# Kernel tuning notes

Measured on AMD Instinct MI355X. Metric: run time of the kernel, lower is better.

Reference implementation:

```python
import jax, jax.numpy as jnp
import numpy as np

E = 8        # num_experts
D = 512      # embed_size
H = 8        # attention heads
HD = D // H  # head dim
B, S = 4, 1024


def setup_inputs() -> dict:
    key = jax.random.key(0)
    ks = jax.random.split(key, 16)
    sd = 0.02
    return {
        "x":  jax.random.normal(ks[0], (B, S, D), jnp.float32),
        # per-expert FFN params, stacked over expert dim
        "W1": jax.random.normal(ks[1], (E, D, 4 * D), jnp.float32) * sd,
        "b1": jnp.zeros((E, 4 * D), jnp.float32),
        "W2": jax.random.normal(ks[2], (E, 4 * D, D), jnp.float32) * sd,
        "b2": jnp.zeros((E, D), jnp.float32),
        # MultiheadAttention in_proj (split) and out_proj
        "Wq": jax.random.normal(ks[3], (D, D), jnp.float32) * sd,
        "bq": jnp.zeros((D,), jnp.float32),
        "Wk": jax.random.normal(ks[4], (D, D), jnp.float32) * sd,
        "bk": jnp.zeros((D,), jnp.float32),
        "Wv": jax.random.normal(ks[5], (D, D), jnp.float32) * sd,
        "bv": jnp.zeros((D,), jnp.float32),
        "Wo": jax.random.normal(ks[6], (D, D), jnp.float32) * sd,
        "bo": jnp.zeros((D,), jnp.float32),
        "expert_id": 3,
    }


def reference(x, W1, b1, W2, b2, Wq, bq, Wk, bk, Wv, bv, Wo, bo, expert_id):
    # --- batched per-expert FFN (fuses the Python loop over experts) ---
    # hidden: [B, E, S, 4D]
    hidden = jax.nn.relu(jnp.einsum('bsd,edf->besf', x, W1) + b1[None, :, None, :])
    eo = jnp.einsum('besf,efd->besd', hidden, W2) + b2[None, :, None, :]  # [B,E,S,D]
    eo = eo.transpose(0, 2, 1, 3)  # [B, S, E, D]

    Bs, Ss = x.shape[0], x.shape[1]
    a = eo.reshape(Bs * Ss, E, D)  # [N, E, D]; attention runs over the expert dim

    # --- MultiheadAttention (batch_first), torch semantics ---
    # NOTE: the original passes a FLOAT tril-of-ones attn_mask, which torch ADDS
    # to the scores (it does NOT mask with -inf). We reproduce that faithfully.
    q = (a @ Wq.T + bq).reshape(-1, E, H, HD).transpose(0, 2, 1, 3)  # [N,H,E,hd]
    k = (a @ Wk.T + bk).reshape(-1, E, H, HD).transpose(0, 2, 1, 3)
    v = (a @ Wv.T + bv).reshape(-1, E, H, HD).transpose(0, 2, 1, 3)

    mask = jnp.tril(jnp.ones((E, E), jnp.float32))  # additive float mask
    scores = jnp.einsum('nhed,nhfd->nhef', q, k) / jnp.sqrt(jnp.float32(HD))
    scores = scores + mask[None, None, :, :]
    attn = jax.nn.softmax(scores, axis=-1)
    ctx = jnp.einsum('nhef,nhfd->nhed', attn, v)           # [N,H,E,hd]
    ctx = ctx.transpose(0, 2, 1, 3).reshape(-1, E, D)       # [N,E,D]
    out = ctx @ Wo.T + bo                                   # [N,E,D]

    out = out.reshape(Bs, Ss, E, D)
    return out[:, :, expert_id, :]  # [B, S, D]
```

## Files before the change

kernel.cpp:

```cpp
#include <hip/hip_runtime.h>
#include <hip/hip_bf16.h>

typedef __hip_bfloat16 bf16;
typedef __attribute__((ext_vector_type(4))) float f32x4;
typedef __attribute__((ext_vector_type(8))) short s16x8;

#define N_TOK 4096
#define Dm    512
#define Fm    2048
#define Em    8

__device__ __forceinline__ float bf2f(bf16 v) { return __bfloat162float(v); }
__device__ __forceinline__ bf16  f2bf(float f) { return __float2bfloat16(f); }

#define GL16(g, l)                                                              \
  __builtin_amdgcn_global_load_lds(                                             \
      (const __attribute__((address_space(1))) void*)(g),                       \
      (__attribute__((address_space(3))) void*)(l), 16, 0, 0)

__global__ void cvt_f32_bf16(const float* __restrict__ in, bf16* __restrict__ out, int n4) {
  int i = blockIdx.x * 256 + threadIdx.x;
  if (i >= n4) return;
  float4 v = reinterpret_cast<const float4*>(in)[i];
  bf16 tmp[4] = {f2bf(v.x), f2bf(v.y), f2bf(v.z), f2bf(v.w)};
  __builtin_memcpy(out + (size_t)i * 4, tmp, 8);
}

__global__ void transpose_cvt(const float* __restrict__ in, bf16* __restrict__ out,
                              int R, int C, long inb, long outb) {
  in  += (long)blockIdx.z * inb;
  out += (long)blockIdx.z * outb;
  __shared__ float t[32][33];
  int tx = threadIdx.x & 31, ty = threadIdx.x >> 5;
  int c0 = blockIdx.x * 32, r0 = blockIdx.y * 32;
#pragma unroll
  for (int i = 0; i < 32; i += 8)
    t[ty + i][tx] = in[(long)(r0 + ty + i) * C + c0 + tx];
  __syncthreads();
#pragma unroll
  for (int i = 0; i < 32; i += 8)
    out[(long)(c0 + ty + i) * R + r0 + tx] = f2bf(t[tx][ty + i]);
}

template <bool RELU, bool OUT_BF16>
__global__ __launch_bounds__(512, 2) void gemm256(
    const bf16* __restrict__ A, const bf16* __restrict__ Bt, void* __restrict__ Cout,
    const float* __restrict__ bias, int K, int lda, int ldb, int ldc,
    long abs_, long bbs, long cbs, long biasbs, int gx, int gy) {
  extern __shared__ bf16 lds[];

  int nwg = gridDim.x;
  int id  = blockIdx.x;
  int lid = (id & 7) * (nwg >> 3) + (id >> 3);
  int per = gx * gy;
  int e   = lid / per;
  int rem = lid - e * per;
  int bx  = rem % gx, by = rem / gx;
  int bm  = bx * 256, bn = by * 256;

  A    += (long)e * abs_;
  Bt   += (long)e * bbs;
  bias += (long)e * biasbs;
  long coff = (long)e * cbs;

  int tid  = threadIdx.x;
  int w    = tid >> 6, lane = tid & 63;
  int wm   = w >> 2, wn = w & 3;

  int srow   = lane >> 2;
  int schunk = (lane & 3) ^ ((lane >> 3) & 3);

  const bf16* Ab = A + (long)bm * lda;
  const bf16* Bb = Bt + (long)bn * ldb;

  int nt = K >> 5;

  auto issue = [&](int t) {
    int k0 = t << 5;
    bf16* buf = lds + (t % 3) * 16384;
#pragma unroll
    for (int j = 0; j < 2; ++j) {
      int ch   = j * 8 + w;
      int rowA = ch * 16 + srow;
      GL16(Ab + (long)rowA * lda + k0 + schunk * 8, buf + ch * 512);
      GL16(Bb + (long)rowA * ldb + k0 + schunk * 8, buf + 8192 + ch * 512);
    }
  };

  f32x4 acc[8][4] = {};
  int la = lane & 15, q = lane >> 4;
  int slotr = q ^ ((la >> 1) & 3);

  auto compute = [&](int t) {
    const bf16* Abuf = lds + (t % 3) * 16384;
    const bf16* Bbuf = Abuf + 8192;
    s16x8 af[8], bfr[4];
#pragma unroll
    for (int m = 0; m < 8; ++m) {
      int r = wm * 128 + m * 16 + la;
      af[m] = *reinterpret_cast<const s16x8*>(Abuf + r * 32 + slotr * 8);
    }
#pragma unroll
    for (int n = 0; n < 4; ++n) {
      int r = wn * 64 + n * 16 + la;
      bfr[n] = *reinterpret_cast<const s16x8*>(Bbuf + r * 32 + slotr * 8);
    }
    __builtin_amdgcn_s_setprio(1);
#pragma unroll
    for (int m = 0; m < 8; ++m)
#pragma unroll
      for (int n = 0; n < 4; ++n)
        acc[m][n] = __builtin_amdgcn_mfma_f32_16x16x32_bf16(bfr[n], af[m], acc[m][n], 0, 0, 0);
    __builtin_amdgcn_s_setprio(0);
  };

  issue(0);
  issue(1);

  for (int t = 0; t < nt - 1; ++t) {
    asm volatile("s_waitcnt vmcnt(4)" ::: "memory");
    __builtin_amdgcn_s_barrier();
    asm volatile("" ::: "memory");
    __builtin_amdgcn_sched_barrier(0);
    if (t + 2 < nt) issue(t + 2);
    compute(t);
    __builtin_amdgcn_sched_barrier(0);
  }
  asm volatile("s_waitcnt vmcnt(0)" ::: "memory");
  __builtin_amdgcn_s_barrier();
  asm volatile("" ::: "memory");
  __builtin_amdgcn_sched_barrier(0);
  compute(nt - 1);

  int nbase0 = bn + wn * 64 + q * 4;
#pragma unroll
  for (int m = 0; m < 8; ++m) {
    int gm = bm + wm * 128 + m * 16 + la;
#pragma unroll
    for (int n = 0; n < 4; ++n) {
      int gn = nbase0 + n * 16;
      float4 b4 = *reinterpret_cast<const float4*>(bias + gn);
      float v0 = acc[m][n][0] + b4.x, v1 = acc[m][n][1] + b4.y;
      float v2 = acc[m][n][2] + b4.z, v3 = acc[m][n][3] + b4.w;
      if (RELU) {
        v0 = fmaxf(v0, 0.f); v1 = fmaxf(v1, 0.f);
        v2 = fmaxf(v2, 0.f); v3 = fmaxf(v3, 0.f);
      }
      long idx = coff + (long)gm * ldc + gn;
      if (OUT_BF16) {
        bf16 tmp[4] = {f2bf(v0), f2bf(v1), f2bf(v2), f2bf(v3)};
        __builtin_memcpy((bf16*)Cout + idx, tmp, 8);
      } else {
        float tmp[4] = {v0, v1, v2, v3};
        __builtin_memcpy((float*)Cout + idx, tmp, 16);
      }
    }
  }
}

template <bool RELU, bool OUT_BF16>
__global__ __launch_bounds__(256, 2) void gemm_bt(
    const bf16* __restrict__ A, const bf16* __restrict__ Bt, void* __restrict__ Cout,
    const float* __restrict__ bias, int M, int N, int K, int lda, int ldb, int ldc,
    long abs_, long bbs, long cbs, long biasbs, const int* __restrict__ eid,
    int eid_scale) {
  int e = blockIdx.z;
  A    += (long)e * abs_;
  Bt   += (long)e * bbs;
  bias += (long)e * biasbs;
  long coff = (long)e * cbs;
  if (eid) A += (long)(*eid) * eid_scale;

  __shared__ bf16 As[128 * 32];
  __shared__ bf16 Bs[128 * 32];

  int tid = threadIdx.x;
  int wave = tid >> 6, lane = tid & 63;
  int wm = wave >> 1, wn = wave & 1;
  int bm = blockIdx.x * 128, bn = blockIdx.y * 128;

  int srow  = lane >> 2;
  int skoff = (lane & 3) * 8;

  f32x4 acc[4][4] = {};

  const bf16* Abase = A + (long)bm * lda;
  const bf16* Bbase = Bt + (long)bn * ldb;

  for (int k0 = 0; k0 < K; k0 += 32) {
    __syncthreads();
#pragma unroll
    for (int i = 0; i < 2; i++) {
      int r = wave * 32 + i * 16 + srow;
      GL16(Abase + (long)r * lda + k0 + skoff, As + (wave * 32 + i * 16) * 32);
      GL16(Bbase + (long)r * ldb + k0 + skoff, Bs + (wave * 32 + i * 16) * 32);
    }
    __syncthreads();

    s16x8 af[4], bfr[4];
#pragma unroll
    for (int m = 0; m < 4; m++)
      af[m] = *reinterpret_cast<const s16x8*>(As + (wm * 64 + m * 16 + (lane & 15)) * 32 +
                                              (lane >> 4) * 8);
#pragma unroll
    for (int n = 0; n < 4; n++)
      bfr[n] = *reinterpret_cast<const s16x8*>(Bs + (wn * 64 + n * 16 + (lane & 15)) * 32 +
                                               (lane >> 4) * 8);
#pragma unroll
    for (int m = 0; m < 4; m++)
#pragma unroll
      for (int n = 0; n < 4; n++)
        acc[m][n] = __builtin_amdgcn_mfma_f32_16x16x32_bf16(af[m], bfr[n], acc[m][n], 0, 0, 0);
  }

  int cr = (lane >> 4) * 4, cc = lane & 15;
#pragma unroll
  for (int m = 0; m < 4; m++) {
#pragma unroll
    for (int n = 0; n < 4; n++) {
      int col  = bn + wn * 64 + n * 16 + cc;
      float bv = bias ? bias[col] : 0.0f;
#pragma unroll
      for (int r = 0; r < 4; r++) {
        int row = bm + wm * 64 + m * 16 + cr + r;
        float v = acc[m][n][r] + bv;
        if (RELU) v = fmaxf(v, 0.0f);
        long idx = coff + (long)row * ldc + col;
        if (OUT_BF16)
          ((bf16*)Cout)[idx] = f2bf(v);
        else
          ((float*)Cout)[idx] = v;
      }
    }
  }
}

__global__ __launch_bounds__(256) void attn_kernel(const float* __restrict__ q,
                                                   const bf16* __restrict__ kv,
                                                   bf16* __restrict__ ctx,
                                                   const int* __restrict__ eid) {
  int wave = threadIdx.x >> 6, lane = threadIdx.x & 63;
  int n = blockIdx.x * 4 + wave;
  int h = lane >> 3, f = lane & 7;
  int e3 = *eid;
  const bf16* kvn = kv + (long)n * Em * (2 * Dm);
  const float* qh = q + (long)n * Dm + h * 64;
  const bf16* kf = kvn + f * (2 * Dm) + h * 64;
  float s = 0.f;
#pragma unroll
  for (int j = 0; j < 64; j++) s += qh[j] * bf2f(kf[j]);
  s *= 0.125f;
  s += (f <= e3) ? 1.0f : 0.0f;
  float mx = s;
#pragma unroll
  for (int d = 1; d < 8; d <<= 1) mx = fmaxf(mx, __shfl_xor(mx, d));
  float ex = expf(s - mx);
  float sm = ex;
#pragma unroll
  for (int d = 1; d < 8; d <<= 1) sm += __shfl_xor(sm, d);
  float at = ex / sm;
  int g = f;
  float acc[8] = {0, 0, 0, 0, 0, 0, 0, 0};
#pragma unroll
  for (int f2 = 0; f2 < 8; f2++) {
    float a = __shfl(at, (h << 3) | f2);
    const bf16* vf = kvn + f2 * (2 * Dm) + Dm + h * 64 + g * 8;
#pragma unroll
    for (int j = 0; j < 8; j++) acc[j] += a * bf2f(vf[j]);
  }
  bf16 tmp[8];
#pragma unroll
  for (int j = 0; j < 8; j++) tmp[j] = f2bf(acc[j]);
  __builtin_memcpy(ctx + (long)n * Dm + h * 64 + g * 8, tmp, 16);
}

extern "C" void kernel_launch(void* const* d_in, const int* in_sizes, int n_in,
                              void* d_out, int out_size, void* d_ws, size_t ws_size,
                              hipStream_t stream) {
  const float* x  = (const float*)d_in[0];
  const float* W1 = (const float*)d_in[1];
  const float* b1 = (const float*)d_in[2];
  const float* W2 = (const float*)d_in[3];
  const float* b2 = (const float*)d_in[4];
  const float* Wq = (const float*)d_in[5];
  const float* bq = (const float*)d_in[6];
  const float* Wk = (const float*)d_in[7];
  const float* bk = (const float*)d_in[8];
  const float* Wv = (const float*)d_in[9];
  const float* bv = (const float*)d_in[10];
  const float* Wo = (const float*)d_in[11];
  const float* bo = (const float*)d_in[12];
  const int* eid  = (const int*)d_in[13];

  char* w = (char*)d_ws;
  auto alloc = [&](size_t bytes) {
    char* p = w;
    w += (bytes + 255) & ~(size_t)255;
    return p;
  };
  bf16* xb   = (bf16*)alloc((size_t)N_TOK * Dm * 2);
  bf16* W1t  = (bf16*)alloc((size_t)Em * Fm * Dm * 2);
  bf16* W2t  = (bf16*)alloc((size_t)Em * Dm * Fm * 2);
  bf16* qw   = (bf16*)alloc((size_t)Dm * Dm * 2);
  bf16* kvw  = (bf16*)alloc((size_t)2 * Dm * Dm * 2);
  bf16* ow   = (bf16*)alloc((size_t)Dm * Dm * 2);
  float* bkv = (float*)alloc((size_t)2 * Dm * 4);
  bf16* hid  = (bf16*)alloc((size_t)Em * N_TOK * Fm * 2);
  bf16* eo   = (bf16*)alloc((size_t)N_TOK * Em * Dm * 2);
  bf16* kv   = (bf16*)hid;
  float* qb  = (float*)(hid + (size_t)N_TOK * Em * 2 * Dm);
  bf16* ctxb = (bf16*)(qb + (size_t)N_TOK * Dm);

  hipFuncSetAttribute(reinterpret_cast<const void*>(gemm256<true, true>),
                      hipFuncAttributeMaxDynamicSharedMemorySize, 98304);
  hipFuncSetAttribute(reinterpret_cast<const void*>(gemm256<false, true>),
                      hipFuncAttributeMaxDynamicSharedMemorySize, 98304);

  cvt_f32_bf16<<<(N_TOK * Dm / 4 + 255) / 256, 256, 0, stream>>>(x, xb, N_TOK * Dm / 4);
  transpose_cvt<<<dim3(Fm / 32, Dm / 32, Em), 256, 0, stream>>>(
      W1, W1t, Dm, Fm, (long)Dm * Fm, (long)Fm * Dm);
  transpose_cvt<<<dim3(Dm / 32, Fm / 32, Em), 256, 0, stream>>>(
      W2, W2t, Fm, Dm, (long)Fm * Dm, (long)Dm * Fm);
  int nw4 = Dm * Dm / 4;
  cvt_f32_bf16<<<(nw4 + 255) / 256, 256, 0, stream>>>(Wq, qw, nw4);
  cvt_f32_bf16<<<(nw4 + 255) / 256, 256, 0, stream>>>(Wk, kvw, nw4);
  cvt_f32_bf16<<<(nw4 + 255) / 256, 256, 0, stream>>>(Wv, kvw + (size_t)Dm * Dm, nw4);
  cvt_f32_bf16<<<(nw4 + 255) / 256, 256, 0, stream>>>(Wo, ow, nw4);
  hipMemcpyAsync(bkv, bk, Dm * sizeof(float), hipMemcpyDeviceToDevice, stream);
  hipMemcpyAsync(bkv + Dm, bv, Dm * sizeof(float), hipMemcpyDeviceToDevice, stream);

  gemm256<true, true><<<16 * 8 * Em, 512, 98304, stream>>>(
      xb, W1t, hid, b1, Dm, Dm, Dm, Fm,
      0L, (long)Fm * Dm, (long)N_TOK * Fm, (long)Fm, 16, 8);
  gemm256<false, true><<<16 * 2 * Em, 512, 98304, stream>>>(
      hid, W2t, eo, b2, Fm, Fm, Fm, Em * Dm,
      (long)N_TOK * Fm, (long)Dm * Fm, (long)Dm, (long)Dm, 16, 2);
  gemm256<false, true><<<128 * 4, 512, 98304, stream>>>(
      eo, kvw, kv, bkv, Dm, Dm, Dm, 2 * Dm,
      0L, 0L, 0L, 0L, 128, 4);
  gemm_bt<false, false><<<dim3(N_TOK / 128, Dm / 128, 1), 256, 0, stream>>>(
      eo, qw, qb, bq, N_TOK, Dm, Dm, Em * Dm, Dm, Dm,
      0L, 0L, 0L, 0L, eid, Dm);
  attn_kernel<<<N_TOK / 4, 256, 0, stream>>>(qb, kv, ctxb, eid);
  gemm_bt<false, false><<<dim3(N_TOK / 128, Dm / 128, 1), 256, 0, stream>>>(
      ctxb, ow, (float*)d_out, bo, N_TOK, Dm, Dm, Dm, Dm, Dm,
      0L, 0L, 0L, 0L, nullptr, 0);
}
```

Baseline: 321.6 us.

## Restructure 256x256 GEMM into 8-wave quadrant-interleaved pipeline with 64-wide K tiles

Rewrites the main bf16 GEMM kernel to use K tiles of 64 with double buffering (128KB LDS) instead of K=32 triple buffering. Each iteration splits the 256x256 tile into four quadrants, interleaving LDS fragment reads, half-tile global-to-LDS prefetches and MFMA bursts between barriers so loads overlap compute more finely. The warp-to-output mapping and the XOR swizzle change to match. The larger LDS footprint may limit occupancy to one block per CU, and the extra barriers add sync cost.

```diff
diff --git a/kernel.cpp b/kernel.cpp
--- a/kernel.cpp
+++ b/kernel.cpp
@@ -17,6 +17,12 @@
   __builtin_amdgcn_global_load_lds(                                             \
       (const __attribute__((address_space(1))) void*)(g),                       \
       (__attribute__((address_space(3))) void*)(l), 16, 0, 0)
+
+#define BAR()                                   \
+  do {                                          \
+    __builtin_amdgcn_s_barrier();               \
+    asm volatile("" ::: "memory");              \
+  } while (0)
 
 __global__ void cvt_f32_bf16(const float* __restrict__ in, bf16* __restrict__ out, int n4) {
   int i = blockIdx.x * 256 + threadIdx.x;
@@ -43,7 +49,7 @@
 }
 
 template <bool RELU, bool OUT_BF16>
-__global__ __launch_bounds__(512, 2) void gemm256(
+__global__ __launch_bounds__(512, 2) void gemm8(
     const bf16* __restrict__ A, const bf16* __restrict__ Bt, void* __restrict__ Cout,
     const float* __restrict__ bias, int K, int lda, int ldb, int ldc,
     long abs_, long bbs, long cbs, long biasbs, int gx, int gy) {
@@ -64,81 +70,109 @@
   long coff = (long)e * cbs;
 
   int tid  = threadIdx.x;
-  int w    = tid >> 6, lane = tid & 63;
-  int wm   = w >> 2, wn = w & 3;
-
-  int srow   = lane >> 2;
-  int schunk = (lane & 3) ^ ((lane >> 3) & 3);
+  int wv   = tid >> 6, lane = tid & 63;
+  int wm   = wv >> 2, wn = wv & 3;
 
   const bf16* Ab = A + (long)bm * lda;
   const bf16* Bb = Bt + (long)bn * ldb;
 
-  int nt = K >> 5;
-
-  auto issue = [&](int t) {
-    int k0 = t << 5;
-    bf16* buf = lds + (t % 3) * 16384;
+  int nt = K >> 6;
+
+  auto stageHalf = [&](int t, int isB, int h) {
+    if (t >= nt) return;
+    int k0 = t << 6;
+    bf16* base = lds + (t & 1) * 32768 + isB * 16384 + h * 8192;
+    const bf16* src = isB ? Bb : Ab;
+    int ldx = isB ? ldb : lda;
 #pragma unroll
     for (int j = 0; j < 2; ++j) {
-      int ch   = j * 8 + w;
-      int rowA = ch * 16 + srow;
-      GL16(Ab + (long)rowA * lda + k0 + schunk * 8, buf + ch * 512);
-      GL16(Bb + (long)rowA * ldb + k0 + schunk * 8, buf + 8192 + ch * 512);
+      int Ll = j * 512 + wv * 64 + lane;
+      int gr = h * 128 + (Ll >> 3);
+      int c  = (Ll & 7) ^ (gr & 7);
+      GL16(src + (long)gr * ldx + k0 + c * 8, base + (j * 512 + wv * 64) * 8);
     }
   };
 
   f32x4 acc[8][4] = {};
   int la = lane & 15, q = lane >> 4;
-  int slotr = q ^ ((la >> 1) & 3);
-
-  auto compute = [&](int t) {
-    const bf16* Abuf = lds + (t % 3) * 16384;
-    const bf16* Bbuf = Abuf + 8192;
-    s16x8 af[8], bfr[4];
-#pragma unroll
-    for (int m = 0; m < 8; ++m) {
-      int r = wm * 128 + m * 16 + la;
-      af[m] = *reinterpret_cast<const s16x8*>(Abuf + r * 32 + slotr * 8);
-    }
+  int sl0 = q ^ (la & 7);
+
+  auto readA = [&](s16x8 af[4][2], int t, int mh) {
+    const bf16* Abuf = lds + (t & 1) * 32768;
+#pragma unroll
+    for (int mi = 0; mi < 4; ++mi) {
+      int r = mh * 128 + wm * 64 + mi * 16 + la;
+#pragma unroll
+      for (int kk = 0; kk < 2; ++kk)
+        af[mi][kk] = *reinterpret_cast<const s16x8*>(Abuf + r * 64 + (sl0 ^ (kk * 4)) * 8);
+    }
+  };
+  auto readB = [&](s16x8 bfv[2][2], int t, int nh) {
+    const bf16* Bbuf = lds + (t & 1) * 32768 + 16384;
+#pragma unroll
+    for (int ni = 0; ni < 2; ++ni) {
+      int r = nh * 128 + wn * 32 + ni * 16 + la;
+#pragma unroll
+      for (int kk = 0; kk < 2; ++kk)
+        bfv[ni][kk] = *reinterpret_cast<const s16x8*>(Bbuf + r * 64 + (sl0 ^ (kk * 4)) * 8);
+    }
+  };
+  auto mfmaQ = [&](int mh, int nh, s16x8 af[4][2], s16x8 bfv[2][2]) {
+    __builtin_amdgcn_s_setprio(1);
+#pragma unroll
+    for (int mi = 0; mi < 4; ++mi)
+#pragma unroll
+      for (int ni = 0; ni < 2; ++ni)
+#pragma unroll
+        for (int kk = 0; kk < 2; ++kk)
+          acc[mh * 4 + mi][nh * 2 + ni] = __builtin_amdgcn_mfma_f32_16x16x32_bf16(
+              bfv[ni][kk], af[mi][kk], acc[mh * 4 + mi][nh * 2 + ni], 0, 0, 0);
+    __builtin_amdgcn_s_setprio(0);
+  };
+
+  stageHalf(0, 0, 0);
+  stageHalf(0, 1, 0);
+  stageHalf(0, 1, 1);
+  stageHalf(0, 0, 1);
+  asm volatile("s_waitcnt vmcnt(4)" ::: "memory");
+  BAR();
+
+  s16x8 af[4][2], b0[2][2], b1[2][2];
+  for (int t = 0; t < nt; ++t) {
+    bool pf = (t + 1 < nt);
+    readA(af, t, 0);
+    readB(b0, t, 0);
+    stageHalf(t + 1, 0, 0);
+    if (pf) asm volatile("s_waitcnt vmcnt(4)" ::: "memory");
+    else    asm volatile("s_waitcnt vmcnt(2)" ::: "memory");
+    BAR();
+    mfmaQ(0, 0, af, b0);
+    BAR();
+    readB(b1, t, 1);
+    stageHalf(t + 1, 1, 0);
+    if (pf) asm volatile("s_waitcnt vmcnt(4)" ::: "memory");
+    else    asm volatile("s_waitcnt vmcnt(0)" ::: "memory");
+    BAR();
+    mfmaQ(0, 1, af, b1);
+    BAR();
+    readA(af, t, 1);
+    stageHalf(t + 1, 1, 1);
+    BAR();
+    mfmaQ(1, 0, af, b0);
+    BAR();
+    stageHalf(t + 1, 0, 1);
+    if (pf) asm volatile("s_waitcnt vmcnt(4)" ::: "memory");
+    BAR();
+    mfmaQ(1, 1, af, b1);
+    BAR();
+  }
+
+#pragma unroll
+  for (int m = 0; m < 8; ++m) {
+    int gm = bm + (m >> 2) * 128 + wm * 64 + (m & 3) * 16 + la;
 #pragma unroll
     for (int n = 0; n < 4; ++n) {
-      int r = wn * 64 + n * 16 + la;
-      bfr[n] = *reinterpret_cast<const s16x8*>(Bbuf + r * 32 + slotr * 8);
-    }
-    __builtin_amdgcn_s_setprio(1);
-#pragma unroll
-    for (int m = 0; m < 8; ++m)
-#pragma unroll
-      for (int n = 0; n < 4; ++n)
-        acc[m][n] = __builtin_amdgcn_mfma_f32_16x16x32_bf16(bfr[n], af[m], acc[m][n], 0, 0, 0);
-    __builtin_amdgcn_s_setprio(0);
-  };
-
-  issue(0);
-  issue(1);
-
-  for (int t = 0; t < nt - 1; ++t) {
-    asm volatile("s_waitcnt vmcnt(4)" ::: "memory");
-    __builtin_amdgcn_s_barrier();
-    asm volatile("" ::: "memory");
-    __builtin_amdgcn_sched_barrier(0);
-    if (t + 2 < nt) issue(t + 2);
-    compute(t);
-    __builtin_amdgcn_sched_barrier(0);
-  }
-  asm volatile("s_waitcnt vmcnt(0)" ::: "memory");
-  __builtin_amdgcn_s_barrier();
-  asm volatile("" ::: "memory");
-  __builtin_amdgcn_sched_barrier(0);
-  compute(nt - 1);
-
-  int nbase0 = bn + wn * 64 + q * 4;
-#pragma unroll
-  for (int m = 0; m < 8; ++m) {
-    int gm = bm + wm * 128 + m * 16 + la;
-#pragma unroll
-    for (int n = 0; n < 4; ++n) {
-      int gn = nbase0 + n * 16;
+      int gn = bn + (n >> 1) * 128 + wn * 32 + (n & 1) * 16 + q * 4;
       float4 b4 = *reinterpret_cast<const float4*>(bias + gn);
       float v0 = acc[m][n][0] + b4.x, v1 = acc[m][n][1] + b4.y;
       float v2 = acc[m][n][2] + b4.z, v3 = acc[m][n][3] + b4.w;
@@ -311,10 +345,10 @@
   float* qb  = (float*)(hid + (size_t)N_TOK * Em * 2 * Dm);
   bf16* ctxb = (bf16*)(qb + (size_t)N_TOK * Dm);
 
-  hipFuncSetAttribute(reinterpret_cast<const void*>(gemm256<true, true>),
-                      hipFuncAttributeMaxDynamicSharedMemorySize, 98304);
-  hipFuncSetAttribute(reinterpret_cast<const void*>(gemm256<false, true>),
-                      hipFuncAttributeMaxDynamicSharedMemorySize, 98304);
+  hipFuncSetAttribute(reinterpret_cast<const void*>(gemm8<true, true>),
+                      hipFuncAttributeMaxDynamicSharedMemorySize, 131072);
+  hipFuncSetAttribute(reinterpret_cast<const void*>(gemm8<false, true>),
+                      hipFuncAttributeMaxDynamicSharedMemorySize, 131072);
 
   cvt_f32_bf16<<<(N_TOK * Dm / 4 + 255) / 256, 256, 0, stream>>>(x, xb, N_TOK * Dm / 4);
   transpose_cvt<<<dim3(Fm / 32, Dm / 32, Em), 256, 0, stream>>>(
@@ -329,13 +363,13 @@
   hipMemcpyAsync(bkv, bk, Dm * sizeof(float), hipMemcpyDeviceToDevice, stream);
   hipMemcpyAsync(bkv + Dm, bv, Dm * sizeof(float), hipMemcpyDeviceToDevice, stream);
 
-  gemm256<true, true><<<16 * 8 * Em, 512, 98304, stream>>>(
+  gemm8<true, true><<<16 * 8 * Em, 512, 131072, stream>>>(
       xb, W1t, hid, b1, Dm, Dm, Dm, Fm,
       0L, (long)Fm * Dm, (long)N_TOK * Fm, (long)Fm, 16, 8);
-  gemm256<false, true><<<16 * 2 * Em, 512, 98304, stream>>>(
+  gemm8<false, true><<<16 * 2 * Em, 512, 131072, stream>>>(
       hid, W2t, eo, b2, Fm, Fm, Fm, Em * Dm,
       (long)N_TOK * Fm, (long)Dm * Fm, (long)Dm, (long)Dm, 16, 2);
-  gemm256<false, true><<<128 * 4, 512, 98304, stream>>>(
+  gemm8<false, true><<<128 * 4, 512, 131072, stream>>>(
       eo, kvw, kv, bkv, Dm, Dm, Dm, 2 * Dm,
       0L, 0L, 0L, 0L, 128, 4);
   gemm_bt<false, false><<<dim3(N_TOK / 128, Dm / 128, 1), 256, 0, stream>>>(
```

After: 316.7 us. Within noise of the previous version (-1.5%).
